# Kernel tuning notes

Hardware: AMD Instinct MI355X
Metric: run time of the kernel (lower is better)

The kernel has to match this reference:

```python
import jax, jax.numpy as jnp
import numpy as np
from jax import lax

B_COEF = 0.25  # commitment loss weight
NUM_EMB = 1024
EMB_DIM = 64


def setup_inputs() -> dict:
    key = jax.random.key(0)
    k1, k2 = jax.random.split(key)
    z_e = jax.random.normal(k1, (32, EMB_DIM, 64, 64), dtype=jnp.float32)
    # codebook init: uniform(-1/num_emb, 1/num_emb) as in torch module
    emb = jax.random.uniform(k2, (NUM_EMB, EMB_DIM), dtype=jnp.float32,
                             minval=-1.0 / NUM_EMB, maxval=1.0 / NUM_EMB)
    return {"z_e": z_e, "emb": emb}


def reference(z_e, emb):
    b, c, h, w = z_e.shape  # c == emb_dim
    # (b,c,h,w) -> (b*h*w, c)
    z_flat = jnp.transpose(z_e, (0, 2, 3, 1)).reshape(b * h * w, c)
    # squared euclidean distance: ||z||^2 + ||e||^2 - 2 z.e^T
    dist = (jnp.sum(z_flat ** 2, axis=-1, keepdims=True)
            + jnp.sum(emb ** 2, axis=-1)[None, :]
            - 2.0 * jnp.matmul(z_flat, emb.T))
    enc_idx = jnp.argmin(dist, axis=-1)  # [b*h*w]
    z_q = emb[enc_idx].reshape(b, h, w, c)  # gather
    z_q = jnp.transpose(z_q, (0, 3, 1, 2))  # (b,c,h,w)
    reconstruction_loss = jnp.mean((z_q - lax.stop_gradient(z_e)) ** 2)
    commitment_loss = B_COEF * jnp.mean((lax.stop_gradient(z_q) - z_e) ** 2)
    loss = reconstruction_loss + commitment_loss
    # straight-through estimator
    z_q_st = z_e + lax.stop_gradient(z_q - z_e)
    return z_q_st, loss, enc_idx
```

## Files before the change

### kernel.cpp

```cpp
#include <hip/hip_runtime.h>
#include <hip/hip_bf16.h>

#define NUM_EMB 1024
#define EMB_DIM 64
#define NPIX    131072
#define ZQ_ELEMS 8388608
#define KDEPTH  16
#define ZSTRIDE 65
#define NACC    64
#define BIAS    0.25f
#define PXB     128
#define NPG     8


typedef __attribute__((ext_vector_type(8))) short short8_t;
typedef __attribute__((ext_vector_type(4))) float f32x4;

__device__ __forceinline__ unsigned umin32(unsigned a, unsigned b) { return a < b ? a : b; }
__device__ __forceinline__ unsigned umed3(unsigned a, unsigned b, unsigned c) {
    unsigned r;
    asm("v_med3_u32 %0, %1, %2, %3" : "=v"(r) : "v"(a), "v"(b), "v"(c));
    return r;
}

__device__ __forceinline__ float np_sumsq64(const float* __restrict__ x) {
    float q[EMB_DIM];
    #pragma unroll
    for (int c = 0; c < EMB_DIM; ++c) q[c] = x[c] * x[c];
    float r0 = q[0], r1 = q[1], r2 = q[2], r3 = q[3];
    float r4 = q[4], r5 = q[5], r6 = q[6], r7 = q[7];
    #pragma unroll
    for (int g = 1; g < 8; ++g) {
        r0 += q[8 * g + 0]; r1 += q[8 * g + 1];
        r2 += q[8 * g + 2]; r3 += q[8 * g + 3];
        r4 += q[8 * g + 4]; r5 += q[8 * g + 5];
        r6 += q[8 * g + 6]; r7 += q[8 * g + 7];
    }
    return ((r0 + r1) + (r2 + r3)) + ((r4 + r5) + (r6 + r7));
}

__device__ __forceinline__ unsigned long long packvk(float v, int k) {
    unsigned u = __float_as_uint(v);
    u = (u & 0x80000000u) ? ~u : (u | 0x80000000u);
    return ((unsigned long long)u << 32) | (unsigned)k;
}

__device__ __forceinline__ float np_score(const float* __restrict__ emb, int k,
                                          const float* __restrict__ zl,
                                          float zzv, float e2k) {
    const float4* ek4 = (const float4*)(emb + k * EMB_DIM);
    float acc = 0.f;
    #pragma unroll
    for (int c4 = 0; c4 < 16; ++c4) {
        float4 e4 = ek4[c4];
        acc = fmaf(e4.x, zl[c4 * 4 + 0], acc);
        acc = fmaf(e4.y, zl[c4 * 4 + 1], acc);
        acc = fmaf(e4.z, zl[c4 * 4 + 2], acc);
        acc = fmaf(e4.w, zl[c4 * 4 + 3], acc);
    }
    return (zzv + e2k) - 2.0f * acc;
}

__global__ __launch_bounds__(256) void vq_prep(const float* __restrict__ emb,
                                               short* __restrict__ wsE,
                                               float* __restrict__ wsE2,
                                               float* __restrict__ wsAcc) {
    #pragma clang fp contract(off)
    int t = blockIdx.x * 256 + threadIdx.x;
    if (blockIdx.x == 0 && threadIdx.x < NACC) wsAcc[threadIdx.x] = 0.f;
    int tt   = t >> 1;
    int h    = t & 1;
    int l    = tt & 63;
    int ch   = (tt >> 6) & 15;
    int q    = tt >> 10;
    int code = q * 256 + ch * 16 + (l & 15);
    const float* ek = emb + code * EMB_DIM;
    short8_t pk;
    #pragma unroll
    for (int j = 0; j < 8; ++j) {
        int chan = 32 * h + 8 * (l >> 4) + j;
        __hip_bfloat16 bv = __float2bfloat16(-2.0f * ek[chan]);
        unsigned short u; __builtin_memcpy(&u, &bv, 2);
        pk[j] = (short)u;
    }
    *(short8_t*)(wsE + tt * 16 + h * 8) = pk;
    if (t < NUM_EMB) wsE2[t] = np_sumsq64(emb + t * EMB_DIM);
}

__global__ __launch_bounds__(256, 3) void vq_mfma(const float* __restrict__ z_e,
                                                  const float* __restrict__ emb,
                                                  const short* __restrict__ wsE,
                                                  const float* __restrict__ wsE2,
                                                  float* __restrict__ zq_out,
                                                  float* __restrict__ enc_out,
                                                  float* __restrict__ wsAcc) {
    #pragma clang fp contract(off)
    __shared__ float sZf[PXB * ZSTRIDE];
    __shared__ float sE2[NUM_EMB];
    __shared__ unsigned sMinP[4][PXB];
    __shared__ float sBand[PXB];
    __shared__ float sThrF[PXB];
    __shared__ unsigned sThrP[PXB];
    __shared__ float sZZ[PXB];
    __shared__ unsigned long long sBestPack[PXB];
    __shared__ unsigned short sKbuf[PXB][KDEPTH];
    __shared__ int   sKcnt[PXB];
    __shared__ int   sPxFlag[PXB];
    __shared__ int   sFlagAny;

    const int tid  = threadIdx.x;
    const int w    = tid >> 6;
    const int lane = tid & 63;
    const int p0   = blockIdx.x * PXB;
    const int b    = p0 >> 12;
    const int hw0  = p0 & 4095;
    const float* base = z_e + (size_t)b * (EMB_DIM * 4096) + hw0;

    *(f32x4*)&sE2[tid * 4] = *(const f32x4*)&wsE2[tid * 4];
    if (tid < PXB) { sKcnt[tid] = 0; sBestPack[tid] = ~0ULL; sPxFlag[tid] = 0; }
    if (tid == 0) sFlagAny = 0;

    {
        const int px = tid & (PXB - 1);
        const int cg = tid >> 7;
        const float* zp = base + px;
        float v[32];
        #pragma unroll
        for (int j = 0; j < 32; ++j) v[j] = zp[(size_t)(32 * cg + j) * 4096];
        #pragma unroll
        for (int j = 0; j < 32; ++j) sZf[px * ZSTRIDE + 32 * cg + j] = v[j];
    }
    __syncthreads();

    if (tid < PXB) {
        const float* zl = &sZf[tid * ZSTRIDE];
        float rr[8] = {0,0,0,0,0,0,0,0};
        float sab = 0.f;
        #pragma unroll
        for (int g = 0; g < 8; ++g)
            #pragma unroll
            for (int j = 0; j < 8; ++j) {
                float zc = zl[8 * g + j];
                float qq = zc * zc;
                rr[j] += qq;
                sab += fabsf(zc);
            }
        sZZ[tid]   = ((rr[0] + rr[1]) + (rr[2] + rr[3])) + ((rr[4] + rr[5]) + (rr[6] + rr[7]));
        sBand[tid] = 2.0f * (9e-6f * sab + 2e-5f) + 1e-4f;
    }

    short8_t bfrag[NPG][2];
    #pragma unroll
    for (int pg = 0; pg < NPG; ++pg)
        #pragma unroll
        for (int h = 0; h < 2; ++h) {
            int bpr = pg * 16 + (lane & 15);
            int c0  = 32 * h + 8 * (lane >> 4);
            short8_t pk;
            #pragma unroll
            for (int j = 0; j < 8; ++j) {
                __hip_bfloat16 bv = __float2bfloat16(sZf[bpr * ZSTRIDE + c0 + j]);
                unsigned short u; __builtin_memcpy(&u, &bv, 2);
                pk[j] = (short)u;
            }
            asm volatile("" : "+v"(pk));
            bfrag[pg][h] = pk;
        }

    const short8_t* ef = (const short8_t*)wsE + (size_t)w * 2048;

    unsigned p1[NPG], p2[NPG], p3[NPG];
    #pragma unroll
    for (int pg = 0; pg < NPG; ++pg) { p1[pg] = ~0u; p2[pg] = ~0u; p3[pg] = ~0u; }
    {
        short8_t A0a = ef[(0 * 64 + lane) * 2 + 0];
        short8_t A1a = ef[(0 * 64 + lane) * 2 + 1];
        short8_t A0b = ef[(1 * 64 + lane) * 2 + 0];
        short8_t A1b = ef[(1 * 64 + lane) * 2 + 1];
        #pragma unroll 1
        for (int ch = 0; ch < 16; ch += 2) {
            {
                int chn = ch + 2 < 16 ? ch + 2 : 15;
                short8_t N0 = ef[(chn * 64 + lane) * 2 + 0];
                short8_t N1 = ef[(chn * 64 + lane) * 2 + 1];
                int kbase = w * 256 + ch * 16 + 4 * (lane >> 4);
                f32x4 e2v = *(const f32x4*)(&sE2[kbase]);
                f32x4 e2bv;
                e2bv[0] = e2v[0] + BIAS; e2bv[1] = e2v[1] + BIAS;
                e2bv[2] = e2v[2] + BIAS; e2bv[3] = e2v[3] + BIAS;
                unsigned kb[4] = {(unsigned)kbase, (unsigned)kbase + 1u,
                                  (unsigned)kbase + 2u, (unsigned)kbase + 3u};
                #pragma unroll
                for (int pg = 0; pg < NPG; ++pg) {
                    f32x4 acc = __builtin_amdgcn_mfma_f32_16x16x32_bf16(A0a, bfrag[pg][0], e2bv, 0, 0, 0);
                    acc = __builtin_amdgcn_mfma_f32_16x16x32_bf16(A1a, bfrag[pg][1], acc, 0, 0, 0);
                    #pragma unroll
                    for (int j = 0; j < 4; ++j) {
                        unsigned t   = (__float_as_uint(acc[j]) & 0xFFFFFC00u) | kb[j];
                        unsigned np2 = umed3(p1[pg], p2[pg], t);
                        unsigned np3 = umed3(p2[pg], p3[pg], t);
                        p1[pg] = umin32(p1[pg], t);
                        p2[pg] = np2; p3[pg] = np3;
                    }
                }
                A0a = N0; A1a = N1;
            }
            {
                int chn = ch + 3 < 16 ? ch + 3 : 15;
                short8_t N0 = ef[(chn * 64 + lane) * 2 + 0];
                short8_t N1 = ef[(chn * 64 + lane) * 2 + 1];
                int kbase = w * 256 + (ch + 1) * 16 + 4 * (lane >> 4);
                f32x4 e2v = *(const f32x4*)(&sE2[kbase]);
                f32x4 e2bv;
                e2bv[0] = e2v[0] + BIAS; e2bv[1] = e2v[1] + BIAS;
                e2bv[2] = e2v[2] + BIAS; e2bv[3] = e2v[3] + BIAS;
                unsigned kb[4] = {(unsigned)kbase, (unsigned)kbase + 1u,
                                  (unsigned)kbase + 2u, (unsigned)kbase + 3u};
                #pragma unroll
                for (int pg = 0; pg < NPG; ++pg) {
                    f32x4 acc = __builtin_amdgcn_mfma_f32_16x16x32_bf16(A0b, bfrag[pg][0], e2bv, 0, 0, 0);
                    acc = __builtin_amdgcn_mfma_f32_16x16x32_bf16(A1b, bfrag[pg][1], acc, 0, 0, 0);
                    #pragma unroll
                    for (int j = 0; j < 4; ++j) {
                        unsigned t   = (__float_as_uint(acc[j]) & 0xFFFFFC00u) | kb[j];
                        unsigned np2 = umed3(p1[pg], p2[pg], t);
                        unsigned np3 = umed3(p2[pg], p3[pg], t);
                        p1[pg] = umin32(p1[pg], t);
                        p2[pg] = np2; p3[pg] = np3;
                    }
                }
                A0b = N0; A1b = N1;
            }
        }
    }

    #pragma unroll
    for (int pg = 0; pg < NPG; ++pg) {
        unsigned g = p1[pg];
        g = umin32(g, (unsigned)__shfl_xor((int)g, 16, 64));
        g = umin32(g, (unsigned)__shfl_xor((int)g, 32, 64));
        if (lane < 16) sMinP[w][pg * 16 + lane] = g;
    }
    __syncthreads();
    if (tid < PXB) {
        unsigned gp = umin32(umin32(sMinP[0][tid], sMinP[1][tid]),
                             umin32(sMinP[2][tid], sMinP[3][tid]));
        float m    = __uint_as_float(gp & 0xFFFFFC00u);
        float thrF = m + sBand[tid];
        sThrF[tid] = thrF;
        sThrP[tid] = (__float_as_uint(thrF) & 0xFFFFFC00u) | 1023u;
    }
    __syncthreads();

    #pragma unroll
    for (int pg = 0; pg < NPG; ++pg) {
        int px = pg * 16 + (lane & 15);
        unsigned thrp = sThrP[px];
        int n = (p1[pg] <= thrp) + (p2[pg] <= thrp) + (p3[pg] <= thrp);
        if (n) {
            int slot = atomicAdd(&sKcnt[px], n);
            if (slot < KDEPTH)                     sKbuf[px][slot]     = (unsigned short)(p1[pg] & 1023u);
            if (n >= 2 && slot + 1 < KDEPTH)       sKbuf[px][slot + 1] = (unsigned short)(p2[pg] & 1023u);
            if (n >= 3) {
                if (slot + 2 < KDEPTH)             sKbuf[px][slot + 2] = (unsigned short)(p3[pg] & 1023u);
                sPxFlag[px] = 1; sFlagAny = 1;
            }
        }
    }
    __syncthreads();

    if (sFlagAny) {
        if (tid < PXB && sPxFlag[tid]) sKcnt[tid] = 0;
        __syncthreads();
        float thrB[NPG];
        #pragma unroll
        for (int pg = 0; pg < NPG; ++pg) {
            int px = pg * 16 + (lane & 15);
            thrB[pg] = sPxFlag[px] ? sThrF[px] : -1e30f;
        }
        short8_t A0 = ef[lane * 2 + 0];
        short8_t A1 = ef[lane * 2 + 1];
        #pragma unroll 1
        for (int ch = 0; ch < 16; ++ch) {
            int chn = ch < 15 ? ch + 1 : 15;
            short8_t N0 = ef[(chn * 64 + lane) * 2 + 0];
            short8_t N1 = ef[(chn * 64 + lane) * 2 + 1];
            int kbase = w * 256 + ch * 16 + 4 * (lane >> 4);
            f32x4 e2v = *(const f32x4*)(&sE2[kbase]);
            f32x4 e2bv;
            e2bv[0] = e2v[0] + BIAS; e2bv[1] = e2v[1] + BIAS;
            e2bv[2] = e2v[2] + BIAS; e2bv[3] = e2v[3] + BIAS;
            #pragma unroll
            for (int pg = 0; pg < NPG; ++pg) {
                f32x4 acc = __builtin_amdgcn_mfma_f32_16x16x32_bf16(A0, bfrag[pg][0], e2bv, 0, 0, 0);
                acc = __builtin_amdgcn_mfma_f32_16x16x32_bf16(A1, bfrag[pg][1], acc, 0, 0, 0);
                #pragma unroll
                for (int j = 0; j < 4; ++j) {
                    if (acc[j] <= thrB[pg]) {
                        int pix  = pg * 16 + (lane & 15);
                        int slot = atomicAdd(&sKcnt[pix], 1);
                        if (slot < KDEPTH) sKbuf[pix][slot] = (unsigned short)(kbase + j);
                    }
                }
            }
            A0 = N0; A1 = N1;
        }
        __syncthreads();
    }

    {
        const int px   = tid & (PXB - 1);
        const int half = tid >> 7;
        const float* zl = &sZf[px * ZSTRIDE];
        float zzv = sZZ[px];
        int rawcnt = sKcnt[px];
        if (rawcnt == 1) {
            if (half == 0) sBestPack[px] = packvk(-1e30f, (int)sKbuf[px][0]);
        } else if (rawcnt <= KDEPTH) {
            for (int s = half; s < rawcnt; s += 2) {
                int k = (int)sKbuf[px][s];
                float v = np_score(emb, k, zl, zzv, sE2[k]);
                atomicMin(&sBestPack[px], packvk(v, k));
            }
        } else {
            for (int k = half; k < NUM_EMB; k += 2) {
                float v = np_score(emb, k, zl, zzv, sE2[k]);
                atomicMin(&sBestPack[px], packvk(v, k));
            }
        }
    }
    __syncthreads();

    if (tid < PXB)
        enc_out[p0 + tid] = (float)(unsigned)(sBestPack[tid] & 0xFFFFFFFFull);
    {
        const int px   = tid & (PXB - 1);
        const int cg   = tid >> 7;
        int bestk = (int)(sBestPack[px] & 0xFFFFFFFFull);
        const float4* eq4 = (const float4*)(emb + bestk * EMB_DIM) + 8 * cg;
        const float* zl = &sZf[px * ZSTRIDE];
        float* op = zq_out + (size_t)b * (EMB_DIM * 4096) + hw0 + px;
        float ls = 0.f;
        #pragma unroll
        for (int j4 = 0; j4 < 8; ++j4) {
            float4 e4 = eq4[j4];
            int c = 32 * cg + j4 * 4;
            float d0 = e4.x - zl[c + 0];
            float d1 = e4.y - zl[c + 1];
            float d2 = e4.z - zl[c + 2];
            float d3 = e4.w - zl[c + 3];
            ls = fmaf(d0, d0, ls);
            ls = fmaf(d1, d1, ls);
            ls = fmaf(d2, d2, ls);
            ls = fmaf(d3, d3, ls);
            op[(size_t)(c + 0) * 4096] = e4.x;
            op[(size_t)(c + 1) * 4096] = e4.y;
            op[(size_t)(c + 2) * 4096] = e4.z;
            op[(size_t)(c + 3) * 4096] = e4.w;
        }
        #pragma unroll
        for (int off = 32; off > 0; off >>= 1) ls += __shfl_down(ls, off, 64);
        if (lane == 0) atomicAdd(&wsAcc[blockIdx.x & (NACC - 1)], ls);
    }
}

__global__ void vq_final_ws(const float* __restrict__ wsAcc,
                            float* __restrict__ loss_out) {
    int lane = threadIdx.x;
    float v = wsAcc[lane];
    #pragma unroll
    for (int off = 32; off > 0; off >>= 1) v += __shfl_down(v, off, 64);
    if (lane == 0) loss_out[0] = v * (1.25f / (float)ZQ_ELEMS);
}

__global__ void vq_final_direct(float* __restrict__ loss_out) {
    loss_out[0] = loss_out[0] * (1.25f / (float)ZQ_ELEMS);
}

__global__ __launch_bounds__(256) void vq_nn_fb(const float* __restrict__ z_e,
                                                const float* __restrict__ emb,
                                                float* __restrict__ zq_out,
                                                float* __restrict__ enc_out,
                                                float* __restrict__ loss_acc) {
    #pragma clang fp contract(off)
    __shared__ float s_e2[NUM_EMB];
    int tid = threadIdx.x;
    for (int k = tid; k < NUM_EMB; k += 256) s_e2[k] = np_sumsq64(emb + k * EMB_DIM);
    __syncthreads();
    int p = blockIdx.x * 256 + tid;
    int b = p >> 12, hw = p & 4095;
    const float* zp = z_e + (size_t)b * (EMB_DIM * 4096) + hw;
    float z[EMB_DIM];
    #pragma unroll
    for (int c = 0; c < EMB_DIM; ++c) z[c] = zp[(size_t)c * 4096];
    float zz = np_sumsq64(z);
    float b1 = 3.4e38f; int i1 = 0;
    #pragma unroll 2
    for (int k = 0; k < NUM_EMB; ++k) {
        const float* ek = emb + k * EMB_DIM;
        float acc = 0.f;
        #pragma unroll
        for (int c = 0; c < EMB_DIM; ++c) acc = fmaf(ek[c], z[c], acc);
        float sc = (zz + s_e2[k]) - 2.0f * acc;
        bool lt = sc < b1; b1 = lt ? sc : b1; i1 = lt ? k : i1;
    }
    const float* eq = emb + i1 * EMB_DIM;
    float* op = zq_out + (size_t)b * (EMB_DIM * 4096) + hw;
    float ls = 0.f;
    #pragma unroll
    for (int c = 0; c < EMB_DIM; ++c) {
        float q = eq[c]; float d = q - z[c];
        ls = fmaf(d, d, ls);
        op[(size_t)c * 4096] = q;
    }
    enc_out[p] = (float)i1;
    #pragma unroll
    for (int off = 32; off > 0; off >>= 1) ls += __shfl_down(ls, off, 64);
    if ((tid & 63) == 0) atomicAdd(loss_acc, ls);
}

extern "C" void kernel_launch(void* const* d_in, const int* in_sizes, int n_in,
                              void* d_out, int out_size, void* d_ws, size_t ws_size,
                              hipStream_t stream) {
    const float* z_e = (const float*)d_in[0];
    const float* emb = (const float*)d_in[1];
    float* out = (float*)d_out;
    float* loss_out = out + ZQ_ELEMS;
    float* enc_out  = out + ZQ_ELEMS + 1;

    if (ws_size >= 140 * 1024) {
        short* wsE   = (short*)d_ws;
        float* wsE2  = (float*)((char*)d_ws + 131072);
        float* wsAcc = (float*)((char*)d_ws + 135168);
        vq_prep<<<32, 256, 0, stream>>>(emb, wsE, wsE2, wsAcc);
        vq_mfma<<<NPIX / PXB, 256, 0, stream>>>(z_e, emb, wsE, wsE2, out, enc_out, wsAcc);
        vq_final_ws<<<1, 64, 0, stream>>>(wsAcc, loss_out);
    } else {
        hipMemsetAsync(loss_out, 0, 4, stream);
        vq_nn_fb<<<NPIX / 256, 256, 0, stream>>>(z_e, emb, out, enc_out, loss_out);
        vq_final_direct<<<1, 1, 0, stream>>>(loss_out);
    }
}
```

Measured before the change: 76.55 us.

## Shrink shared memory to raise vq_mfma occupancy from 3 to 4 blocks

```diff
diff --git a/kernel.cpp b/kernel.cpp
--- a/kernel.cpp
+++ b/kernel.cpp
@@ -64,6 +64,7 @@
 __global__ __launch_bounds__(256) void vq_prep(const float* __restrict__ emb,
                                                short* __restrict__ wsE,
                                                float* __restrict__ wsE2,
+                                               float* __restrict__ wsE2b,
                                                float* __restrict__ wsAcc) {
     #pragma clang fp contract(off)
     int t = blockIdx.x * 256 + threadIdx.x;
@@ -84,28 +85,29 @@
         pk[j] = (short)u;
     }
     *(short8_t*)(wsE + tt * 16 + h * 8) = pk;
-    if (t < NUM_EMB) wsE2[t] = np_sumsq64(emb + t * EMB_DIM);
-}
-
-__global__ __launch_bounds__(256, 3) void vq_mfma(const float* __restrict__ z_e,
+    if (t < NUM_EMB) {
+        float e2 = np_sumsq64(emb + t * EMB_DIM);
+        wsE2[t]  = e2;
+        wsE2b[t] = e2 + BIAS;
+    }
+}
+
+__global__ __launch_bounds__(256, 4) void vq_mfma(const float* __restrict__ z_e,
                                                   const float* __restrict__ emb,
                                                   const short* __restrict__ wsE,
                                                   const float* __restrict__ wsE2,
+                                                  const float* __restrict__ wsE2b,
                                                   float* __restrict__ zq_out,
                                                   float* __restrict__ enc_out,
                                                   float* __restrict__ wsAcc) {
     #pragma clang fp contract(off)
     __shared__ float sZf[PXB * ZSTRIDE];
-    __shared__ float sE2[NUM_EMB];
-    __shared__ unsigned sMinP[4][PXB];
-    __shared__ float sBand[PXB];
-    __shared__ float sThrF[PXB];
-    __shared__ unsigned sThrP[PXB];
-    __shared__ float sZZ[PXB];
+    __shared__ unsigned sMinP[PXB];
+    __shared__ float sThr[PXB];
     __shared__ unsigned long long sBestPack[PXB];
     __shared__ unsigned short sKbuf[PXB][KDEPTH];
     __shared__ int   sKcnt[PXB];
-    __shared__ int   sPxFlag[PXB];
+    __shared__ unsigned short sPxFlag[PXB];
     __shared__ int   sFlagAny;
 
     const int tid  = threadIdx.x;
@@ -116,8 +118,10 @@
     const int hw0  = p0 & 4095;
     const float* base = z_e + (size_t)b * (EMB_DIM * 4096) + hw0;
 
-    *(f32x4*)&sE2[tid * 4] = *(const f32x4*)&wsE2[tid * 4];
-    if (tid < PXB) { sKcnt[tid] = 0; sBestPack[tid] = ~0ULL; sPxFlag[tid] = 0; }
+    if (tid < PXB) {
+        sKcnt[tid] = 0; sBestPack[tid] = ~0ULL; sPxFlag[tid] = 0;
+        sMinP[tid] = ~0u;
+    }
     if (tid == 0) sFlagAny = 0;
 
     {
@@ -134,19 +138,10 @@
 
     if (tid < PXB) {
         const float* zl = &sZf[tid * ZSTRIDE];
-        float rr[8] = {0,0,0,0,0,0,0,0};
         float sab = 0.f;
         #pragma unroll
-        for (int g = 0; g < 8; ++g)
-            #pragma unroll
-            for (int j = 0; j < 8; ++j) {
-                float zc = zl[8 * g + j];
-                float qq = zc * zc;
-                rr[j] += qq;
-                sab += fabsf(zc);
-            }
-        sZZ[tid]   = ((rr[0] + rr[1]) + (rr[2] + rr[3])) + ((rr[4] + rr[5]) + (rr[6] + rr[7]));
-        sBand[tid] = 2.0f * (9e-6f * sab + 2e-5f) + 1e-4f;
+        for (int c = 0; c < EMB_DIM; ++c) sab += fabsf(zl[c]);
+        sThr[tid] = 2.0f * (9e-6f * sab + 2e-5f) + 1e-4f;
     }
 
     short8_t bfrag[NPG][2];
@@ -184,10 +179,7 @@
                 short8_t N0 = ef[(chn * 64 + lane) * 2 + 0];
                 short8_t N1 = ef[(chn * 64 + lane) * 2 + 1];
                 int kbase = w * 256 + ch * 16 + 4 * (lane >> 4);
-                f32x4 e2v = *(const f32x4*)(&sE2[kbase]);
-                f32x4 e2bv;
-                e2bv[0] = e2v[0] + BIAS; e2bv[1] = e2v[1] + BIAS;
-                e2bv[2] = e2v[2] + BIAS; e2bv[3] = e2v[3] + BIAS;
+                f32x4 e2bv = *(const f32x4*)(wsE2b + kbase);
                 unsigned kb[4] = {(unsigned)kbase, (unsigned)kbase + 1u,
                                   (unsigned)kbase + 2u, (unsigned)kbase + 3u};
                 #pragma unroll
@@ -210,10 +202,7 @@
                 short8_t N0 = ef[(chn * 64 + lane) * 2 + 0];
                 short8_t N1 = ef[(chn * 64 + lane) * 2 + 1];
                 int kbase = w * 256 + (ch + 1) * 16 + 4 * (lane >> 4);
-                f32x4 e2v = *(const f32x4*)(&sE2[kbase]);
-                f32x4 e2bv;
-                e2bv[0] = e2v[0] + BIAS; e2bv[1] = e2v[1] + BIAS;
-                e2bv[2] = e2v[2] + BIAS; e2bv[3] = e2v[3] + BIAS;
+                f32x4 e2bv = *(const f32x4*)(wsE2b + kbase);
                 unsigned kb[4] = {(unsigned)kbase, (unsigned)kbase + 1u,
                                   (unsigned)kbase + 2u, (unsigned)kbase + 3u};
                 #pragma unroll
@@ -239,23 +228,19 @@
         unsigned g = p1[pg];
         g = umin32(g, (unsigned)__shfl_xor((int)g, 16, 64));
         g = umin32(g, (unsigned)__shfl_xor((int)g, 32, 64));
-        if (lane < 16) sMinP[w][pg * 16 + lane] = g;
+        if (lane < 16) atomicMin(&sMinP[pg * 16 + lane], g);
     }
     __syncthreads();
     if (tid < PXB) {
-        unsigned gp = umin32(umin32(sMinP[0][tid], sMinP[1][tid]),
-                             umin32(sMinP[2][tid], sMinP[3][tid]));
-        float m    = __uint_as_float(gp & 0xFFFFFC00u);
-        float thrF = m + sBand[tid];
-        sThrF[tid] = thrF;
-        sThrP[tid] = (__float_as_uint(thrF) & 0xFFFFFC00u) | 1023u;
+        float m = __uint_as_float(sMinP[tid] & 0xFFFFFC00u);
+        sThr[tid] = m + sThr[tid];
     }
     __syncthreads();
 
     #pragma unroll
     for (int pg = 0; pg < NPG; ++pg) {
         int px = pg * 16 + (lane & 15);
-        unsigned thrp = sThrP[px];
+        unsigned thrp = (__float_as_uint(sThr[px]) & 0xFFFFFC00u) | 1023u;
         int n = (p1[pg] <= thrp) + (p2[pg] <= thrp) + (p3[pg] <= thrp);
         if (n) {
             int slot = atomicAdd(&sKcnt[px], n);
@@ -276,7 +261,7 @@
         #pragma unroll
         for (int pg = 0; pg < NPG; ++pg) {
             int px = pg * 16 + (lane & 15);
-            thrB[pg] = sPxFlag[px] ? sThrF[px] : -1e30f;
+            thrB[pg] = sPxFlag[px] ? sThr[px] : -1e30f;
         }
         short8_t A0 = ef[lane * 2 + 0];
         short8_t A1 = ef[lane * 2 + 1];
@@ -286,10 +271,7 @@
             short8_t N0 = ef[(chn * 64 + lane) * 2 + 0];
             short8_t N1 = ef[(chn * 64 + lane) * 2 + 1];
             int kbase = w * 256 + ch * 16 + 4 * (lane >> 4);
-            f32x4 e2v = *(const f32x4*)(&sE2[kbase]);
-            f32x4 e2bv;
-            e2bv[0] = e2v[0] + BIAS; e2bv[1] = e2v[1] + BIAS;
-            e2bv[2] = e2v[2] + BIAS; e2bv[3] = e2v[3] + BIAS;
+            f32x4 e2bv = *(const f32x4*)(wsE2b + kbase);
             #pragma unroll
             for (int pg = 0; pg < NPG; ++pg) {
                 f32x4 acc = __builtin_amdgcn_mfma_f32_16x16x32_bf16(A0, bfrag[pg][0], e2bv, 0, 0, 0);
@@ -312,19 +294,20 @@
         const int px   = tid & (PXB - 1);
         const int half = tid >> 7;
         const float* zl = &sZf[px * ZSTRIDE];
-        float zzv = sZZ[px];
         int rawcnt = sKcnt[px];
         if (rawcnt == 1) {
             if (half == 0) sBestPack[px] = packvk(-1e30f, (int)sKbuf[px][0]);
         } else if (rawcnt <= KDEPTH) {
+            float zzv = np_sumsq64(zl);
             for (int s = half; s < rawcnt; s += 2) {
                 int k = (int)sKbuf[px][s];
-                float v = np_score(emb, k, zl, zzv, sE2[k]);
+                float v = np_score(emb, k, zl, zzv, wsE2[k]);
                 atomicMin(&sBestPack[px], packvk(v, k));
             }
         } else {
+            float zzv = np_sumsq64(zl);
             for (int k = half; k < NUM_EMB; k += 2) {
-                float v = np_score(emb, k, zl, zzv, sE2[k]);
+                float v = np_score(emb, k, zl, zzv, wsE2[k]);
                 atomicMin(&sBestPack[px], packvk(v, k));
             }
         }
@@ -431,9 +414,11 @@
     if (ws_size >= 140 * 1024) {
         short* wsE   = (short*)d_ws;
         float* wsE2  = (float*)((char*)d_ws + 131072);
-        float* wsAcc = (float*)((char*)d_ws + 135168);
-        vq_prep<<<32, 256, 0, stream>>>(emb, wsE, wsE2, wsAcc);
-        vq_mfma<<<NPIX / PXB, 256, 0, stream>>>(z_e, emb, wsE, wsE2, out, enc_out, wsAcc);
+        float* wsE2b = (float*)((char*)d_ws + 135168);
+        float* wsAcc = (float*)((char*)d_ws + 139264);
+        vq_prep<<<32, 256, 0, stream>>>(emb, wsE, wsE2, wsE2b, wsAcc);
+        vq_mfma<<<NPIX / PXB, 256, 0, stream>>>(z_e, emb, wsE, wsE2, wsE2b,
+                                                out, enc_out, wsAcc);
         vq_final_ws<<<1, 64, 0, stream>>>(wsAcc, loss_out);
     } else {
         hipMemsetAsync(loss_out, 0, 4, stream);
```

Result: slower. 79.47 us (+3.8%).
